# Kernel tuning notes

Measured on AMD Instinct MI355X. Metric: run time of the kernel, lower is better.

Reference implementation:

```python
import jax, jax.numpy as jnp
import numpy as np

B, S, E, H = 2, 4096, 512, 8
DK = E // H


def setup_inputs() -> dict:
    k = jax.random.key(0)
    ks = jax.random.split(k, 11)
    sc = 0.02
    return {
        "query": jax.random.normal(ks[0], (B, S, E), jnp.float32),
        "key_in": jax.random.normal(ks[1], (B, S, E), jnp.float32),
        "value": jax.random.normal(ks[2], (B, S, E), jnp.float32),
        "Wq": jax.random.normal(ks[3], (E, E), jnp.float32) * sc,
        "bq": jax.random.normal(ks[4], (E,), jnp.float32) * sc,
        "Wk": jax.random.normal(ks[5], (E, E), jnp.float32) * sc,
        "bk": jax.random.normal(ks[6], (E,), jnp.float32) * sc,
        "Wv": jax.random.normal(ks[7], (E, E), jnp.float32) * sc,
        "bv": jax.random.normal(ks[8], (E,), jnp.float32) * sc,
        "Wo": jax.random.normal(ks[9], (E, E), jnp.float32) * sc,
        "bo": jax.random.normal(ks[10], (E,), jnp.float32) * sc,
    }


def reference(query, key_in, value, Wq, bq, Wk, bk, Wv, bv, Wo, bo):
    b, s, _ = query.shape
    # Linear projections
    q = query @ Wq + bq
    k = key_in @ Wk + bk
    v = value @ Wv + bv
    # [b, s, H, dk] -> [b, H, s, dk]
    q = q.reshape(b, s, H, DK).transpose(0, 2, 1, 3)
    k = k.reshape(b, s, H, DK).transpose(0, 2, 1, 3)
    v = v.reshape(b, s, H, DK).transpose(0, 2, 1, 3)
    # NOTE: source bug — softmax over UNSCALED scores (1/sqrt scaling in the
    # original is applied to a dead variable after softmax). Reproduce faithfully.
    scores = jnp.einsum("bhqd,bhkd->bhqk", q, k)  # [b,H,s,s] — O(N^2) materialized
    weights = jax.nn.softmax(scores.astype(jnp.float32), axis=-1)
    attn = jnp.einsum("bhqk,bhkd->bhqd", weights, v)
    # [b,H,s,dk] -> [b,s,E]
    concat = attn.transpose(0, 2, 1, 3).reshape(b, s, E)
    return concat @ Wo + bo
```

## Files before the change

### kernel.cpp

```cpp
#include <hip/hip_runtime.h>
#include <hip/hip_bf16.h>

#define B_  2
#define S_  4096
#define E_  512
#define H_  8
#define DK_ 64
#define M_  8192

typedef float f32x4  __attribute__((ext_vector_type(4)));
typedef float f32x16 __attribute__((ext_vector_type(16)));
typedef short s16x8  __attribute__((ext_vector_type(8)));
typedef short s16x4  __attribute__((ext_vector_type(4)));

static __device__ __forceinline__ short f2bf(float x) {
  __hip_bfloat16 h = __float2bfloat16(x);
  return __builtin_bit_cast(short, h);
}

static __device__ __forceinline__ f32x4 mfma32(s16x8 a, s16x8 b, f32x4 c) {
  return __builtin_amdgcn_mfma_f32_16x16x32_bf16(a, b, c, 0, 0, 0);
}

static __device__ __forceinline__ f32x16 mfma3232(s16x8 a, s16x8 b, f32x16 c) {
  return __builtin_amdgcn_mfma_f32_32x32x16_bf16(a, b, c, 0, 0, 0);
}

static __device__ __forceinline__ void gload_lds16(const void* g, void* l) {
  __builtin_amdgcn_global_load_lds(
      (const __attribute__((address_space(1))) unsigned int*)g,
      (__attribute__((address_space(3))) unsigned int*)l, 16, 0, 0);
}

static __device__ __forceinline__ int swz(int row, int colByte) {
  return row * 128 + (colByte ^ ((row & 7) << 4));
}

__global__ __launch_bounds__(256) void conv_bf16(const float* __restrict__ in,
                                                 short* __restrict__ out, int n4) {
  int i = blockIdx.x * 256 + threadIdx.x;
  if (i < n4) {
    float4 v = *((const float4*)in + i);
    s16x4 o;
    o[0] = f2bf(v.x); o[1] = f2bf(v.y); o[2] = f2bf(v.z); o[3] = f2bf(v.w);
    *((s16x4*)out + i) = o;
  }
}

__global__ __launch_bounds__(256) void conv_wT(const float* __restrict__ W,
                                               short* __restrict__ Wt) {
  int idx = blockIdx.x * 256 + threadIdx.x;
  int j = idx >> 9, k = idx & 511;
  Wt[idx] = f2bf(W[(size_t)k * E_ + j]);
}

static __device__ __forceinline__ void gemm_core_512(
    const short* __restrict__ A, const short* __restrict__ Bt,
    short* As, short* Bs, int tm, int tn, f32x4 acc[4][4]) {
  const int tid = threadIdx.x;
  const int wave = tid >> 6, lane = tid & 63;
  const int wm = (wave >> 1) * 64, wn = (wave & 1) * 64;
  const int c = lane & 15, g = lane >> 4;
  for (int kk = 0; kk < 512; kk += 64) {
#pragma unroll
    for (int i = 0; i < 4; ++i) {
      int ob = wave * 4096 + i * 1024 + lane * 16;
      int row = ob >> 7;
      int col = (ob & 127) >> 1;
      gload_lds16(A + (size_t)(tm + row) * 512 + kk + col,
                  (char*)As + wave * 4096 + i * 1024);
      gload_lds16(Bt + (size_t)(tn + row) * 512 + kk + col,
                  (char*)Bs + wave * 4096 + i * 1024);
    }
    __syncthreads();
#pragma unroll
    for (int s = 0; s < 2; ++s) {
      s16x8 af[4], bfr[4];
#pragma unroll
      for (int i = 0; i < 4; ++i)
        af[i] = *(const s16x8*)&As[(wm + i * 16 + c) * 64 + s * 32 + g * 8];
#pragma unroll
      for (int j = 0; j < 4; ++j)
        bfr[j] = *(const s16x8*)&Bs[(wn + j * 16 + c) * 64 + s * 32 + g * 8];
#pragma unroll
      for (int i = 0; i < 4; ++i)
#pragma unroll
        for (int j = 0; j < 4; ++j)
          acc[i][j] = mfma32(af[i], bfr[j], acc[i][j]);
    }
    __syncthreads();
  }
}

__global__ __launch_bounds__(256) void gemm_qkv(
    const short* __restrict__ Xq, const short* __restrict__ Xk,
    const short* __restrict__ Xv, const short* __restrict__ Wt,
    const float* __restrict__ bq, const float* __restrict__ bk,
    const float* __restrict__ bv,
    short* __restrict__ Qo, short* __restrict__ Ko, short* __restrict__ Vto) {
  __shared__ __align__(16) short As[128 * 64];
  __shared__ __align__(16) short Bs[128 * 64];
  const int z = blockIdx.z;
  const short* A = (z == 0) ? Xq : ((z == 1) ? Xk : Xv);
  const short* Bt = Wt + z * (E_ * E_);
  const float* bias = (z == 0) ? bq : ((z == 1) ? bk : bv);
  const int tm = blockIdx.x * 128, tn = blockIdx.y * 128;
  f32x4 acc[4][4] = {};
  gemm_core_512(A, Bt, As, Bs, tm, tn, acc);

  const int tid = threadIdx.x;
  const int wave = tid >> 6, lane = tid & 63;
  const int wm = (wave >> 1) * 64, wn = (wave & 1) * 64;
  const int c = lane & 15, g = lane >> 4;
#pragma unroll
  for (int i = 0; i < 4; ++i) {
#pragma unroll
    for (int j = 0; j < 4; ++j) {
      const int gc = tn + wn + j * 16 + c;
      const float bb = bias[gc];
      const int h = gc >> 6, dk = gc & 63;
#pragma unroll
      for (int r = 0; r < 4; ++r) {
        const int gr = tm + wm + i * 16 + g * 4 + r;
        const int b = gr >> 12, s = gr & 4095;
        const short hv = f2bf(acc[i][j][r] + bb);
        if (z == 2)
          Vto[(size_t)((b * H_ + h) * DK_ + dk) * S_ + s] = hv;
        else if (z == 1)
          Ko[(size_t)((b * H_ + h) * S_ + s) * DK_ + dk] = hv;
        else
          Qo[(size_t)((b * H_ + h) * S_ + s) * DK_ + dk] = hv;
      }
    }
  }
}

__global__ __launch_bounds__(256) void gemm_out(
    const short* __restrict__ AO, const short* __restrict__ Wot,
    const float* __restrict__ bo, float* __restrict__ out) {
  __shared__ __align__(16) short As[128 * 64];
  __shared__ __align__(16) short Bs[128 * 64];
  const int tm = blockIdx.x * 128, tn = blockIdx.y * 128;
  f32x4 acc[4][4] = {};
  gemm_core_512(AO, Wot, As, Bs, tm, tn, acc);

  const int tid = threadIdx.x;
  const int wave = tid >> 6, lane = tid & 63;
  const int wm = (wave >> 1) * 64, wn = (wave & 1) * 64;
  const int c = lane & 15, g = lane >> 4;
#pragma unroll
  for (int i = 0; i < 4; ++i) {
#pragma unroll
    for (int j = 0; j < 4; ++j) {
      const int gc = tn + wn + j * 16 + c;
      const float bb = bo[gc];
#pragma unroll
      for (int r = 0; r < 4; ++r) {
        const int gr = tm + wm + i * 16 + g * 4 + r;
        out[(size_t)gr * E_ + gc] = acc[i][j][r] + bb;
      }
    }
  }
}

__global__ __launch_bounds__(256, 2) void attn_fwd(
    const short* __restrict__ Q, const short* __restrict__ K,
    const short* __restrict__ Vt, short* __restrict__ O) {
  __shared__ __align__(16) short Ks[2][64 * 64];
  __shared__ __align__(16) short Vs[2][64 * 64];
  const int tid = threadIdx.x;
  const int wave = tid >> 6, lane = tid & 63;
  const int qi = lane & 31, hi = lane >> 5;
  const int bh = blockIdx.y;
  const int b = bh >> 3, h = bh & 7;
  const int q0 = blockIdx.x * 128 + wave * 32;
  const short* Qp = Q + (size_t)bh * S_ * DK_;
  const short* Kp = K + (size_t)bh * S_ * DK_;
  const short* Vp = Vt + (size_t)bh * DK_ * S_;

  s16x8 qf[4];
#pragma unroll
  for (int s = 0; s < 4; ++s)
    qf[s] = *(const s16x8*)(Qp + (size_t)(q0 + qi) * DK_ + s * 16 + hi * 8);

  f32x16 o0 = {}, o1 = {};
  f32x16 lacc = {};
  s16x8 ones;
#pragma unroll
  for (int e = 0; e < 8; ++e) ones[e] = (short)0x3F80;

  auto stage = [&](int kt, int buf) {
    const int k0 = kt * 64;
#pragma unroll
    for (int r = 0; r < 2; ++r) {
      const int ob = wave * 2048 + r * 1024 + (lane << 4);
      const int row = ob >> 7;
      const int cbl = (ob & 127) ^ ((row & 7) << 4);
      const int srow = (row & 32) | ((row & 8) << 1) | ((row & 4) << 1) |
                       ((row & 16) >> 2) | (row & 3);
      gload_lds16(Kp + (size_t)(k0 + srow) * DK_ + (cbl >> 1),
                  (char*)Ks[buf] + wave * 2048 + r * 1024);
      gload_lds16(Vp + (size_t)row * S_ + k0 + (cbl >> 1),
                  (char*)Vs[buf] + wave * 2048 + r * 1024);
    }
  };

  stage(0, 0);
  __syncthreads();

  const int NT = S_ / 64;
  for (int kt = 0; kt < NT; ++kt) {
    const int cur = kt & 1;
    if (kt + 1 < NT) stage(kt + 1, cur ^ 1);
    const char* Kc = (const char*)Ks[cur];
    const char* Vc = (const char*)Vs[cur];

    f32x16 s0 = {}, s1 = {};
    __builtin_amdgcn_s_setprio(1);
#pragma unroll
    for (int s = 0; s < 4; ++s) {
      s16x8 ka = *(const s16x8*)(Kc + swz(qi, s * 32 + hi * 16));
      s16x8 kb = *(const s16x8*)(Kc + swz(32 + qi, s * 32 + hi * 16));
      s0 = mfma3232(ka, qf[s], s0);
      s1 = mfma3232(kb, qf[s], s1);
    }
    __builtin_amdgcn_s_setprio(0);

    float p0[16], p1[16];
#pragma unroll
    for (int r = 0; r < 16; ++r) { p0[r] = __expf(s0[r]); p1[r] = __expf(s1[r]); }

    s16x8 pb[2][2];
#pragma unroll
    for (int ks = 0; ks < 2; ++ks)
#pragma unroll
      for (int j = 0; j < 8; ++j) {
        const int r = (j & 3) | (ks << 2) | ((j >> 2) << 3);
        pb[0][ks][j] = f2bf(p0[r]);
        pb[1][ks][j] = f2bf(p1[r]);
      }

    __builtin_amdgcn_s_setprio(1);
#pragma unroll
    for (int half = 0; half < 2; ++half)
#pragma unroll
      for (int ks = 0; ks < 2; ++ks) {
        s16x8 va0 = *(const s16x8*)(Vc + swz(qi, half * 64 + ks * 32 + hi * 16));
        s16x8 va1 = *(const s16x8*)(Vc + swz(32 + qi, half * 64 + ks * 32 + hi * 16));
        o0 = mfma3232(va0, pb[half][ks], o0);
        o1 = mfma3232(va1, pb[half][ks], o1);
        lacc = mfma3232(ones, pb[half][ks], lacc);
      }
    __builtin_amdgcn_s_setprio(0);

    __syncthreads();
  }

  const float rl = 1.f / lacc[0];
  short* Op = O + ((size_t)(b * S_ + q0 + qi)) * E_ + h * DK_;
#pragma unroll
  for (int rr = 0; rr < 4; ++rr) {
    s16x4 ov0, ov1;
#pragma unroll
    for (int e = 0; e < 4; ++e) {
      ov0[e] = f2bf(o0[rr * 4 + e] * rl);
      ov1[e] = f2bf(o1[rr * 4 + e] * rl);
    }
    *(s16x4*)(Op + rr * 8 + hi * 4) = ov0;
    *(s16x4*)(Op + 32 + rr * 8 + hi * 4) = ov1;
  }
}

extern "C" void kernel_launch(void* const* d_in, const int* in_sizes, int n_in,
                              void* d_out, int out_size, void* d_ws, size_t ws_size,
                              hipStream_t stream) {
  const float* query  = (const float*)d_in[0];
  const float* key_in = (const float*)d_in[1];
  const float* value  = (const float*)d_in[2];
  const float* Wq = (const float*)d_in[3];
  const float* bq = (const float*)d_in[4];
  const float* Wk = (const float*)d_in[5];
  const float* bk = (const float*)d_in[6];
  const float* Wv = (const float*)d_in[7];
  const float* bv = (const float*)d_in[8];
  const float* Wo = (const float*)d_in[9];
  const float* bo = (const float*)d_in[10];
  float* out = (float*)d_out;

  const size_t NA = (size_t)M_ * E_;
  short* ws  = (short*)d_ws;
  short* Xq  = ws;
  short* Xk  = Xq + NA;
  short* Xv  = Xk + NA;
  short* Wt  = Xv + NA;
  short* Wot = Wt + 3 * E_ * E_;
  short* Qb  = Wot + E_ * E_;
  short* Kb  = Qb + NA;
  short* Vtb = Kb + NA;
  short* AO  = Vtb + NA;

  conv_bf16<<<dim3(NA / 1024), 256, 0, stream>>>(query, Xq, (int)(NA / 4));
  conv_bf16<<<dim3(NA / 1024), 256, 0, stream>>>(key_in, Xk, (int)(NA / 4));
  conv_bf16<<<dim3(NA / 1024), 256, 0, stream>>>(value, Xv, (int)(NA / 4));
  conv_wT<<<dim3(E_ * E_ / 256), 256, 0, stream>>>(Wq, Wt);
  conv_wT<<<dim3(E_ * E_ / 256), 256, 0, stream>>>(Wk, Wt + E_ * E_);
  conv_wT<<<dim3(E_ * E_ / 256), 256, 0, stream>>>(Wv, Wt + 2 * E_ * E_);
  conv_wT<<<dim3(E_ * E_ / 256), 256, 0, stream>>>(Wo, Wot);

  gemm_qkv<<<dim3(M_ / 128, E_ / 128, 3), 256, 0, stream>>>(
      Xq, Xk, Xv, Wt, bq, bk, bv, Qb, Kb, Vtb);
  attn_fwd<<<dim3(S_ / 128, B_ * H_), 256, 0, stream>>>(Qb, Kb, Vtb, AO);
  gemm_out<<<dim3(M_ / 128, E_ / 128), 256, 0, stream>>>(AO, Wot, bo, out);
}
```

Baseline: 178.5 us.

## Software-pipeline QK^T one tile ahead of softmax-PV in attention loop

Restructures the flash-attention main loop so the QK^T MFMA for tile t+1 is issued alongside exp/convert and PV MFMAs for tile t, using a two-step unrolled loop with ping-pong score registers. K and V staging are split, and V gets four LDS buffers so V for a tile stays resident while later tiles are prefetched. The aim is to overlap exp (VALU) work with matrix-core work and hide LDS latency. The cost is extra register pressure from a second set of score accumulators and doubled V LDS, which may hurt occupancy at launch bounds of 2 blocks.

Measured after the change: 177.5 us. Within noise of the previous version (-0.6%).

```diff
diff --git a/kernel.cpp b/kernel.cpp
--- a/kernel.cpp
+++ b/kernel.cpp
@@ -167,7 +167,7 @@
     const short* __restrict__ Q, const short* __restrict__ K,
     const short* __restrict__ Vt, short* __restrict__ O) {
   __shared__ __align__(16) short Ks[2][64 * 64];
-  __shared__ __align__(16) short Vs[2][64 * 64];
+  __shared__ __align__(16) short Vs[4][64 * 64];
   const int tid = threadIdx.x;
   const int wave = tid >> 6, lane = tid & 63;
   const int qi = lane & 31, hi = lane >> 5;
@@ -189,8 +189,7 @@
 #pragma unroll
   for (int e = 0; e < 8; ++e) ones[e] = (short)0x3F80;
 
-  auto stage = [&](int kt, int buf) {
-    const int k0 = kt * 64;
+  auto stageK = [&](int kt, int buf) {
 #pragma unroll
     for (int r = 0; r < 2; ++r) {
       const int ob = wave * 2048 + r * 1024 + (lane << 4);
@@ -198,38 +197,39 @@
       const int cbl = (ob & 127) ^ ((row & 7) << 4);
       const int srow = (row & 32) | ((row & 8) << 1) | ((row & 4) << 1) |
                        ((row & 16) >> 2) | (row & 3);
-      gload_lds16(Kp + (size_t)(k0 + srow) * DK_ + (cbl >> 1),
+      gload_lds16(Kp + (size_t)(kt * 64 + srow) * DK_ + (cbl >> 1),
                   (char*)Ks[buf] + wave * 2048 + r * 1024);
-      gload_lds16(Vp + (size_t)row * S_ + k0 + (cbl >> 1),
+    }
+  };
+  auto stageV = [&](int kt, int buf) {
+#pragma unroll
+    for (int r = 0; r < 2; ++r) {
+      const int ob = wave * 2048 + r * 1024 + (lane << 4);
+      const int row = ob >> 7;
+      const int cbl = (ob & 127) ^ ((row & 7) << 4);
+      gload_lds16(Vp + (size_t)row * S_ + kt * 64 + (cbl >> 1),
                   (char*)Vs[buf] + wave * 2048 + r * 1024);
     }
   };
 
-  stage(0, 0);
-  __syncthreads();
-
-  const int NT = S_ / 64;
-  for (int kt = 0; kt < NT; ++kt) {
-    const int cur = kt & 1;
-    if (kt + 1 < NT) stage(kt + 1, cur ^ 1);
-    const char* Kc = (const char*)Ks[cur];
-    const char* Vc = (const char*)Vs[cur];
-
-    f32x16 s0 = {}, s1 = {};
-    __builtin_amdgcn_s_setprio(1);
+  auto qk = [&](const short* Kbuf, f32x16& s0, f32x16& s1) {
+    const char* Kc = (const char*)Kbuf;
+    f32x16 t0 = {}, t1 = {};
 #pragma unroll
     for (int s = 0; s < 4; ++s) {
       s16x8 ka = *(const s16x8*)(Kc + swz(qi, s * 32 + hi * 16));
       s16x8 kb = *(const s16x8*)(Kc + swz(32 + qi, s * 32 + hi * 16));
-      s0 = mfma3232(ka, qf[s], s0);
-      s1 = mfma3232(kb, qf[s], s1);
-    }
-    __builtin_amdgcn_s_setprio(0);
-
+      t0 = mfma3232(ka, qf[s], t0);
+      t1 = mfma3232(kb, qf[s], t1);
+    }
+    s0 = t0; s1 = t1;
+  };
+
+  auto softpv = [&](const f32x16& s0, const f32x16& s1, const short* Vbuf) {
+    const char* Vc = (const char*)Vbuf;
     float p0[16], p1[16];
 #pragma unroll
     for (int r = 0; r < 16; ++r) { p0[r] = __expf(s0[r]); p1[r] = __expf(s1[r]); }
-
     s16x8 pb[2][2];
 #pragma unroll
     for (int ks = 0; ks < 2; ++ks)
@@ -239,7 +239,6 @@
         pb[0][ks][j] = f2bf(p0[r]);
         pb[1][ks][j] = f2bf(p1[r]);
       }
-
     __builtin_amdgcn_s_setprio(1);
 #pragma unroll
     for (int half = 0; half < 2; ++half)
@@ -252,7 +251,25 @@
         lacc = mfma3232(ones, pb[half][ks], lacc);
       }
     __builtin_amdgcn_s_setprio(0);
-
+  };
+
+  const int NT = S_ / 64;
+  f32x16 sA0, sA1, sB0, sB1;
+
+  stageK(0, 0); stageV(0, 0);
+  __syncthreads();
+  stageK(1, 1); stageV(1, 1);
+  qk(Ks[0], sA0, sA1);
+  __syncthreads();
+
+  for (int t = 0; t < NT; t += 2) {
+    if (t + 2 < NT) { stageK(t + 2, t & 1); stageV(t + 2, (t + 2) & 3); }
+    qk(Ks[(t + 1) & 1], sB0, sB1);
+    softpv(sA0, sA1, Vs[t & 3]);
+    __syncthreads();
+    if (t + 3 < NT) { stageK(t + 3, (t + 1) & 1); stageV(t + 3, (t + 3) & 3); }
+    if (t + 2 < NT) qk(Ks[(t + 2) & 1], sA0, sA1);
+    softpv(sB0, sB1, Vs[(t + 1) & 3]);
     __syncthreads();
   }
 
```
